# Kernel optimization log

Measured on AMD Instinct MI355X. Metric: run time of the kernel, lower is better.

The kernel has to match this reference:

```python
import jax, jax.numpy as jnp
import numpy as np
import math

D_MODEL = 96
D_STATE = 16
IMG = 32
KSZ = 3
V_LIST = [(0, 0), (0, 1), (0, -1), (1, 0), (-1, 0)]
NUM_V = len(V_LIST)
GROUPS = 4
BATCH = 4


def group_norm(x, gamma, beta, groups=GROUPS, eps=1e-5):
    B, C, H, W = x.shape
    xg = x.reshape(B, groups, C // groups, H, W)
    mu = xg.mean(axis=(2, 3, 4), keepdims=True)
    var = xg.var(axis=(2, 3, 4), keepdims=True)
    xn = ((xg - mu) * jax.lax.rsqrt(var + eps)).reshape(B, C, H, W)
    return xn * gamma[None, :, None, None] + beta[None, :, None, None]


def circ_conv(x, w, b=None):
    # circular padding then VALID conv == padding_mode='circular'
    p = w.shape[-1] // 2
    xp = jnp.pad(x, ((0, 0), (0, 0), (p, p), (p, p)), mode='wrap')
    y = jax.lax.conv_general_dilated(xp, w, (1, 1), 'VALID',
                                     dimension_numbers=('NCHW', 'OIHW', 'NCHW'))
    if b is not None:
        y = y + b[None, :, None, None]
    return y


def setup_inputs() -> dict:
    key = jax.random.key(0)
    ks = jax.random.split(key, 8)
    fan = D_MODEL * KSZ * KSZ
    inp = {
        'u_t': jax.random.normal(ks[0], (BATCH, D_MODEL, IMG, IMG), jnp.float32),
        's_prev': jax.random.normal(ks[1], (BATCH, NUM_V, D_MODEL, D_STATE, IMG, IMG), jnp.float32) * 0.1,
        'gamma': jnp.ones((D_MODEL,), jnp.float32),
        'beta': jnp.zeros((D_MODEL,), jnp.float32),
        'w_delta': jax.random.normal(ks[2], (D_MODEL, D_MODEL, KSZ, KSZ), jnp.float32) / np.sqrt(fan),
        'b_delta': jnp.zeros((D_MODEL,), jnp.float32),
        'w_B': jax.random.normal(ks[3], (D_STATE, D_MODEL, KSZ, KSZ), jnp.float32) / np.sqrt(fan),
        'w_C': jax.random.normal(ks[4], (D_STATE, D_MODEL, KSZ, KSZ), jnp.float32) / np.sqrt(fan),
        'log_A_real': jnp.full((D_MODEL, D_STATE), math.log(0.5), jnp.float32),
        'D_param': jnp.ones((D_MODEL,), jnp.float32),
        'dt_inv_softplus': jnp.asarray(math.log(math.exp(1.0) - 1.0), jnp.float32),
    }
    return inp


def reference(u_t, s_prev, gamma, beta, w_delta, b_delta, w_B, w_C, log_A_real, D_param, dt_inv_softplus):
    B, D, H, W = u_t.shape
    N = D_STATE
    u_norm = group_norm(u_t, gamma, beta)
    delta = jax.nn.softplus(circ_conv(u_norm, w_delta, b_delta) + dt_inv_softplus)
    delta = jnp.clip(delta, 1e-4, 5.0)                          # (B,D,H,W)
    B_val = circ_conv(u_norm, w_B)                               # (B,N,H,W)
    C_val = circ_conv(u_norm, w_C)                               # (B,N,H,W)
    A = -jnp.exp(log_A_real)                                     # (D,N)
    delta_bc = delta[:, :, None]                                 # (B,D,1,H,W)
    A_bar = jnp.exp(delta_bc * A[None, :, :, None, None])        # (B,D,N,H,W)
    B_bar = delta_bc * B_val[:, None]                            # (B,D,N,H,W)
    # flow transport: dest[y,x] = src[(y-vy)%H,(x-vx)%W] == roll by (vy,vx)
    s_tr = jnp.stack([jnp.roll(s_prev[:, i], shift=v, axis=(-2, -1))
                      for i, v in enumerate(V_LIST)], axis=1)    # (B,V,D,N,H,W)
    s_new = A_bar[:, None] * s_tr + B_bar[:, None] * u_t[:, None, :, None]
    y_state = jnp.sum(s_new * C_val[:, None, None], axis=3)      # (B,V,D,H,W)
    y_out = y_state + u_t[:, None] * D_param[None, None, :, None, None]
    return (y_out, s_new)
```

## Files before the change

kernel.cpp:

```cpp
#include <hip/hip_runtime.h>
#include <math.h>

#define D_MODEL 96
#define D_STATE 16
#define IMG 32
#define NUM_V 5
#define GROUPS 4
#define BATCH 4
#define HW (IMG*IMG)
#define CPG (D_MODEL/GROUPS)
#define NCOEF (D_MODEL + 2*D_STATE)
#define Y_SIZE (BATCH*NUM_V*D_MODEL*HW)

__global__ __launch_bounds__(256) void gn_kernel(const float* __restrict__ u,
                                                 const float* __restrict__ gamma,
                                                 const float* __restrict__ beta,
                                                 float* __restrict__ unorm) {
    int b = blockIdx.x >> 2, g = blockIdx.x & 3;
    int t = threadIdx.x;
    const int base = (b * D_MODEL + g * CPG) * HW;
    const int n = CPG * HW;
    float s = 0.f, s2 = 0.f;
    for (int k = t; k < n; k += 256) {
        float v = u[base + k];
        s += v;
        s2 = fmaf(v, v, s2);
    }
    for (int off = 32; off; off >>= 1) {
        s  += __shfl_down(s,  off);
        s2 += __shfl_down(s2, off);
    }
    __shared__ float red[8];
    int wid = t >> 6;
    if ((t & 63) == 0) { red[wid * 2] = s; red[wid * 2 + 1] = s2; }
    __syncthreads();
    if (t == 0) {
        float S = 0.f, S2 = 0.f;
        for (int i = 0; i < 4; ++i) { S += red[i * 2]; S2 += red[i * 2 + 1]; }
        float mu  = S / (float)n;
        float var = S2 / (float)n - mu * mu;
        red[0] = mu;
        red[1] = rsqrtf(var + 1e-5f);
    }
    __syncthreads();
    float mu = red[0], rs = red[1];
    for (int k = t; k < n; k += 256) {
        int c = g * CPG + (k >> 10);
        unorm[base + k] = (u[base + k] - mu) * rs * gamma[c] + beta[c];
    }
}

__global__ __launch_bounds__(256) void conv_kernel(const float* __restrict__ unorm,
                                                   const float* __restrict__ w_delta,
                                                   const float* __restrict__ b_delta,
                                                   const float* __restrict__ w_B,
                                                   const float* __restrict__ w_C,
                                                   const float* __restrict__ dt_ptr,
                                                   float* __restrict__ coef) {
    int bid = blockIdx.x;
    int b  = bid >> 9;
    int oc = (bid >> 2) & 127;
    int hq = bid & 3;
    int t  = threadIdx.x;
    int h  = hq * 8 + (t >> 5);
    int w  = t & 31;
    int lane    = t & 63;
    int rowBase = lane & 32;
    int lsrc = rowBase | ((lane + 31) & 31);
    int rsrc = rowBase | ((lane + 1) & 31);

    const float* wp;
    float bias;
    bool is_delta = false;
    if (oc < D_MODEL) {
        wp = w_delta + oc * D_MODEL * 9;
        bias = b_delta[oc] + dt_ptr[0];
        is_delta = true;
    } else if (oc < D_MODEL + D_STATE) {
        wp = w_B + (oc - D_MODEL) * D_MODEL * 9;
        bias = 0.f;
    } else {
        wp = w_C + (oc - D_MODEL - D_STATE) * D_MODEL * 9;
        bias = 0.f;
    }
    const float* ub = unorm + b * D_MODEL * HW;

    float acc = bias;
    for (int ic = 0; ic < D_MODEL; ++ic) {
        const float* wr = wp + ic * 9;
        const float* ur = ub + ic * HW;
        #pragma unroll
        for (int kh = 0; kh < 3; ++kh) {
            int hh = (h + kh + 31) & 31;
            float c = ur[hh * 32 + w];
            float l = __shfl(c, lsrc);
            float r = __shfl(c, rsrc);
            acc = fmaf(wr[kh * 3 + 0], l, acc);
            acc = fmaf(wr[kh * 3 + 1], c, acc);
            acc = fmaf(wr[kh * 3 + 2], r, acc);
        }
    }
    if (is_delta) {
        float sp = acc > 20.f ? acc : log1pf(__expf(acc));
        acc = fminf(fmaxf(sp, 1e-4f), 5.f);
    }
    coef[(b * NCOEF + oc) * HW + h * 32 + w] = acc;
}

__global__ __launch_bounds__(256) void state_kernel(const float* __restrict__ u_t,
                                                    const float* __restrict__ s_prev,
                                                    const float* __restrict__ coef,
                                                    const float* __restrict__ log_A,
                                                    const float* __restrict__ D_param,
                                                    float* __restrict__ out) {
    int gid = blockIdx.x * 256 + threadIdx.x;
    int b  = gid / (D_MODEL * HW);
    int r  = gid - b * (D_MODEL * HW);
    int d  = r >> 10;
    int hw = r & 1023;
    int h = hw >> 5, w = hw & 31;

    float delta = coef[(b * NCOEF + d) * HW + hw];
    float u     = u_t[(b * D_MODEL + d) * HW + hw];
    float Dp    = D_param[d];

    float Ab[D_STATE], bu[D_STATE], Cv[D_STATE];
    #pragma unroll
    for (int n = 0; n < D_STATE; ++n) {
        float Bv = coef[(b * NCOEF + D_MODEL + n) * HW + hw];
        Cv[n]    = coef[(b * NCOEF + D_MODEL + D_STATE + n) * HW + hw];
        float A  = -__expf(log_A[d * D_STATE + n]);
        Ab[n]    = __expf(delta * A);
        bu[n]    = delta * Bv * u;
    }

    float* out_s = out + Y_SIZE;
    const int vh[NUM_V] = {0, 0, 0, 1, -1};
    const int vw[NUM_V] = {0, 1, -1, 0, 0};
    #pragma unroll
    for (int i = 0; i < NUM_V; ++i) {
        int hs  = (h - vh[i]) & 31;
        int ws  = (w - vw[i]) & 31;
        int hw2 = hs * 32 + ws;
        long sbase = (long)((b * NUM_V + i) * D_MODEL + d) * (D_STATE * HW);
        float y = 0.f;
        #pragma unroll
        for (int n = 0; n < D_STATE; ++n) {
            float s  = s_prev[sbase + n * HW + hw2];
            float sn = fmaf(Ab[n], s, bu[n]);
            out_s[sbase + n * HW + hw] = sn;
            y = fmaf(sn, Cv[n], y);
        }
        out[(long)((b * NUM_V + i) * D_MODEL + d) * HW + hw] = y + u * Dp;
    }
}

extern "C" void kernel_launch(void* const* d_in, const int* in_sizes, int n_in,
                              void* d_out, int out_size, void* d_ws, size_t ws_size,
                              hipStream_t stream) {
    const float* u_t     = (const float*)d_in[0];
    const float* s_prev  = (const float*)d_in[1];
    const float* gamma   = (const float*)d_in[2];
    const float* beta    = (const float*)d_in[3];
    const float* w_delta = (const float*)d_in[4];
    const float* b_delta = (const float*)d_in[5];
    const float* w_B     = (const float*)d_in[6];
    const float* w_C     = (const float*)d_in[7];
    const float* log_A   = (const float*)d_in[8];
    const float* D_param = (const float*)d_in[9];
    const float* dt_ptr  = (const float*)d_in[10];
    float* out = (float*)d_out;

    float* unorm = (float*)d_ws;
    float* coef  = unorm + BATCH * D_MODEL * HW;

    hipLaunchKernelGGL(gn_kernel, dim3(BATCH * GROUPS), dim3(256), 0, stream,
                       u_t, gamma, beta, unorm);
    hipLaunchKernelGGL(conv_kernel, dim3(BATCH * NCOEF * 4), dim3(256), 0, stream,
                       unorm, w_delta, b_delta, w_B, w_C, dt_ptr, coef);
    hipLaunchKernelGGL(state_kernel, dim3(BATCH * D_MODEL * HW / 256), dim3(256), 0, stream,
                       u_t, s_prev, coef, log_A, D_param, out);
}
```

Measured before the change: 354.9 us.

## Vectorize all kernels with float4 loads/stores and nontemporal state writes

Rewrites the group-norm, conv and state kernels to process four adjacent pixels per thread with float4 loads and stores. Horizontal neighbours come from lane shuffles, and the per-state coefficients are computed inside the n loop instead of being held in register arrays. State outputs use nontemporal stores to avoid polluting cache with the large streaming write. The conv grid shrinks to one block per output channel and batch, which cuts parallelism there and makes each thread do four times the work.

```diff
diff --git a/kernel.cpp b/kernel.cpp
--- a/kernel.cpp
+++ b/kernel.cpp
@@ -12,19 +12,26 @@
 #define NCOEF (D_MODEL + 2*D_STATE)
 #define Y_SIZE (BATCH*NUM_V*D_MODEL*HW)
 
-__global__ __launch_bounds__(256) void gn_kernel(const float* __restrict__ u,
+typedef float f32x4 __attribute__((ext_vector_type(4)));
+
+__device__ __forceinline__ void nt_store4(const float4& v, float4* p) {
+    f32x4 tmp = {v.x, v.y, v.z, v.w};
+    __builtin_nontemporal_store(tmp, (f32x4*)p);
+}
+
+__global__ __launch_bounds__(256) void gn_kernel(const float4* __restrict__ u4,
                                                  const float* __restrict__ gamma,
                                                  const float* __restrict__ beta,
-                                                 float* __restrict__ unorm) {
+                                                 float4* __restrict__ unorm4) {
     int b = blockIdx.x >> 2, g = blockIdx.x & 3;
     int t = threadIdx.x;
-    const int base = (b * D_MODEL + g * CPG) * HW;
-    const int n = CPG * HW;
+    const int base4 = ((b * D_MODEL + g * CPG) * HW) >> 2;
+    const int n4 = (CPG * HW) >> 2;
     float s = 0.f, s2 = 0.f;
-    for (int k = t; k < n; k += 256) {
-        float v = u[base + k];
-        s += v;
-        s2 = fmaf(v, v, s2);
+    for (int k = t; k < n4; k += 256) {
+        float4 v = u4[base4 + k];
+        s += v.x + v.y + v.z + v.w;
+        s2 = fmaf(v.x, v.x, fmaf(v.y, v.y, fmaf(v.z, v.z, fmaf(v.w, v.w, s2))));
     }
     for (int off = 32; off; off >>= 1) {
         s  += __shfl_down(s,  off);
@@ -37,37 +44,41 @@
     if (t == 0) {
         float S = 0.f, S2 = 0.f;
         for (int i = 0; i < 4; ++i) { S += red[i * 2]; S2 += red[i * 2 + 1]; }
-        float mu  = S / (float)n;
-        float var = S2 / (float)n - mu * mu;
+        float nf = (float)(CPG * HW);
+        float mu  = S / nf;
+        float var = S2 / nf - mu * mu;
         red[0] = mu;
         red[1] = rsqrtf(var + 1e-5f);
     }
     __syncthreads();
     float mu = red[0], rs = red[1];
-    for (int k = t; k < n; k += 256) {
-        int c = g * CPG + (k >> 10);
-        unorm[base + k] = (u[base + k] - mu) * rs * gamma[c] + beta[c];
-    }
-}
-
-__global__ __launch_bounds__(256) void conv_kernel(const float* __restrict__ unorm,
+    for (int k = t; k < n4; k += 256) {
+        int c = g * CPG + (k >> 8);
+        float ga = gamma[c] * rs, be = beta[c] - mu * gamma[c] * rs;
+        float4 v = u4[base4 + k];
+        float4 o;
+        o.x = fmaf(v.x, ga, be); o.y = fmaf(v.y, ga, be);
+        o.z = fmaf(v.z, ga, be); o.w = fmaf(v.w, ga, be);
+        unorm4[base4 + k] = o;
+    }
+}
+
+__global__ __launch_bounds__(256) void conv_kernel(const float4* __restrict__ unorm4,
                                                    const float* __restrict__ w_delta,
                                                    const float* __restrict__ b_delta,
                                                    const float* __restrict__ w_B,
                                                    const float* __restrict__ w_C,
                                                    const float* __restrict__ dt_ptr,
-                                                   float* __restrict__ coef) {
+                                                   float4* __restrict__ coef4) {
     int bid = blockIdx.x;
-    int b  = bid >> 9;
-    int oc = (bid >> 2) & 127;
-    int hq = bid & 3;
+    int b  = bid >> 7;
+    int oc = bid & 127;
     int t  = threadIdx.x;
-    int h  = hq * 8 + (t >> 5);
-    int w  = t & 31;
-    int lane    = t & 63;
-    int rowBase = lane & 32;
-    int lsrc = rowBase | ((lane + 31) & 31);
-    int rsrc = rowBase | ((lane + 1) & 31);
+    int h  = t >> 3;
+    int j  = t & 7;
+    int lane = t & 63;
+    int ll = (lane & 56) | ((j + 7) & 7);
+    int rl = (lane & 56) | ((j + 1) & 7);
 
     const float* wp;
     float bias;
@@ -83,75 +94,146 @@
         wp = w_C + (oc - D_MODEL - D_STATE) * D_MODEL * 9;
         bias = 0.f;
     }
-    const float* ub = unorm + b * D_MODEL * HW;
-
-    float acc = bias;
+    const float4* ub4 = unorm4 + ((b * D_MODEL * HW) >> 2);
+
+    float4 acc = {bias, bias, bias, bias};
+    int hm = (h + 31) & 31, hp = (h + 1) & 31;
+    int ro[3] = {hm * 8 + j, h * 8 + j, hp * 8 + j};
+
     for (int ic = 0; ic < D_MODEL; ++ic) {
         const float* wr = wp + ic * 9;
-        const float* ur = ub + ic * HW;
+        const int icb = ic * 256;
         #pragma unroll
         for (int kh = 0; kh < 3; ++kh) {
-            int hh = (h + kh + 31) & 31;
-            float c = ur[hh * 32 + w];
-            float l = __shfl(c, lsrc);
-            float r = __shfl(c, rsrc);
-            acc = fmaf(wr[kh * 3 + 0], l, acc);
-            acc = fmaf(wr[kh * 3 + 1], c, acc);
-            acc = fmaf(wr[kh * 3 + 2], r, acc);
+            float4 q = ub4[icb + ro[kh]];
+            float lw = __shfl(q.w, ll);
+            float rx = __shfl(q.x, rl);
+            float wa = wr[kh * 3 + 0], wb = wr[kh * 3 + 1], wc = wr[kh * 3 + 2];
+            acc.x = fmaf(wa, lw,  fmaf(wb, q.x, fmaf(wc, q.y, acc.x)));
+            acc.y = fmaf(wa, q.x, fmaf(wb, q.y, fmaf(wc, q.z, acc.y)));
+            acc.z = fmaf(wa, q.y, fmaf(wb, q.z, fmaf(wc, q.w, acc.z)));
+            acc.w = fmaf(wa, q.z, fmaf(wb, q.w, fmaf(wc, rx,  acc.w)));
         }
     }
     if (is_delta) {
-        float sp = acc > 20.f ? acc : log1pf(__expf(acc));
-        acc = fminf(fmaxf(sp, 1e-4f), 5.f);
-    }
-    coef[(b * NCOEF + oc) * HW + h * 32 + w] = acc;
-}
-
-__global__ __launch_bounds__(256) void state_kernel(const float* __restrict__ u_t,
-                                                    const float* __restrict__ s_prev,
-                                                    const float* __restrict__ coef,
+        float* a = (float*)&acc;
+        #pragma unroll
+        for (int k = 0; k < 4; ++k) {
+            float x = a[k];
+            float sp = x > 20.f ? x : log1pf(__expf(x));
+            a[k] = fminf(fmaxf(sp, 1e-4f), 5.f);
+        }
+    }
+    coef4[((b * NCOEF + oc) * HW >> 2) + h * 8 + j] = acc;
+}
+
+__global__ __launch_bounds__(128) void state_kernel(const float4* __restrict__ u4,
+                                                    const float4* __restrict__ s_prev4,
+                                                    const float4* __restrict__ coef4,
                                                     const float* __restrict__ log_A,
                                                     const float* __restrict__ D_param,
-                                                    float* __restrict__ out) {
-    int gid = blockIdx.x * 256 + threadIdx.x;
-    int b  = gid / (D_MODEL * HW);
-    int r  = gid - b * (D_MODEL * HW);
-    int d  = r >> 10;
-    int hw = r & 1023;
-    int h = hw >> 5, w = hw & 31;
-
-    float delta = coef[(b * NCOEF + d) * HW + hw];
-    float u     = u_t[(b * D_MODEL + d) * HW + hw];
-    float Dp    = D_param[d];
-
-    float Ab[D_STATE], bu[D_STATE], Cv[D_STATE];
+                                                    float4* __restrict__ out4) {
+    int bid = blockIdx.x;
+    int b = bid / 192;
+    int r = bid - b * 192;
+    int d = r >> 1;
+    int half = r & 1;
+    int t = threadIdx.x;
+    int h = half * 16 + (t >> 3);
+    int j = t & 7;
+    int lane = t & 63;
+    int ll = (lane & 56) | ((j + 7) & 7);
+    int rl = (lane & 56) | ((j + 1) & 7);
+    int hw4 = h * 8 + j;
+
+    float4 delta = coef4[((b * NCOEF + d) * HW >> 2) + hw4];
+    float4 u     = u4[((b * D_MODEL + d) * HW >> 2) + hw4];
+    float Dp     = D_param[d];
+    const float* lA = log_A + d * D_STATE;
+
+    int pb[NUM_V];
     #pragma unroll
+    for (int i = 0; i < NUM_V; ++i)
+        pb[i] = ((b * NUM_V + i) * D_MODEL + d) * (D_STATE * HW / 4);
+    int hm4 = (((h + 31) & 31) * 8) + j;
+    int hp4 = (((h + 1) & 31) * 8) + j;
+
+    float4* outs4 = out4 + (Y_SIZE >> 2);
+
+    float4 y0 = {0,0,0,0}, y1 = {0,0,0,0}, y2 = {0,0,0,0}, y3 = {0,0,0,0}, y4v = {0,0,0,0};
+
+    #pragma unroll 2
     for (int n = 0; n < D_STATE; ++n) {
-        float Bv = coef[(b * NCOEF + D_MODEL + n) * HW + hw];
-        Cv[n]    = coef[(b * NCOEF + D_MODEL + D_STATE + n) * HW + hw];
-        float A  = -__expf(log_A[d * D_STATE + n]);
-        Ab[n]    = __expf(delta * A);
-        bu[n]    = delta * Bv * u;
-    }
-
-    float* out_s = out + Y_SIZE;
-    const int vh[NUM_V] = {0, 0, 0, 1, -1};
-    const int vw[NUM_V] = {0, 1, -1, 0, 0};
+        int n4 = n * (HW / 4);
+        float4 Bv = coef4[((b * NCOEF + D_MODEL + n) * HW >> 2) + hw4];
+        float4 Cv = coef4[((b * NCOEF + D_MODEL + D_STATE + n) * HW >> 2) + hw4];
+        float A = -__expf(lA[n]);
+        float4 Ab, bu;
+        Ab.x = __expf(delta.x * A); Ab.y = __expf(delta.y * A);
+        Ab.z = __expf(delta.z * A); Ab.w = __expf(delta.w * A);
+        bu.x = delta.x * Bv.x * u.x; bu.y = delta.y * Bv.y * u.y;
+        bu.z = delta.z * Bv.z * u.z; bu.w = delta.w * Bv.w * u.w;
+
+        {
+            float4 s = s_prev4[pb[0] + n4 + hw4];
+            float4 sn;
+            sn.x = fmaf(Ab.x, s.x, bu.x); sn.y = fmaf(Ab.y, s.y, bu.y);
+            sn.z = fmaf(Ab.z, s.z, bu.z); sn.w = fmaf(Ab.w, s.w, bu.w);
+            nt_store4(sn, &outs4[pb[0] + n4 + hw4]);
+            y0.x = fmaf(sn.x, Cv.x, y0.x); y0.y = fmaf(sn.y, Cv.y, y0.y);
+            y0.z = fmaf(sn.z, Cv.z, y0.z); y0.w = fmaf(sn.w, Cv.w, y0.w);
+        }
+        {
+            float4 q = s_prev4[pb[1] + n4 + hw4];
+            float lw = __shfl(q.w, ll);
+            float4 s = {lw, q.x, q.y, q.z};
+            float4 sn;
+            sn.x = fmaf(Ab.x, s.x, bu.x); sn.y = fmaf(Ab.y, s.y, bu.y);
+            sn.z = fmaf(Ab.z, s.z, bu.z); sn.w = fmaf(Ab.w, s.w, bu.w);
+            nt_store4(sn, &outs4[pb[1] + n4 + hw4]);
+            y1.x = fmaf(sn.x, Cv.x, y1.x); y1.y = fmaf(sn.y, Cv.y, y1.y);
+            y1.z = fmaf(sn.z, Cv.z, y1.z); y1.w = fmaf(sn.w, Cv.w, y1.w);
+        }
+        {
+            float4 q = s_prev4[pb[2] + n4 + hw4];
+            float rx = __shfl(q.x, rl);
+            float4 s = {q.y, q.z, q.w, rx};
+            float4 sn;
+            sn.x = fmaf(Ab.x, s.x, bu.x); sn.y = fmaf(Ab.y, s.y, bu.y);
+            sn.z = fmaf(Ab.z, s.z, bu.z); sn.w = fmaf(Ab.w, s.w, bu.w);
+            nt_store4(sn, &outs4[pb[2] + n4 + hw4]);
+            y2.x = fmaf(sn.x, Cv.x, y2.x); y2.y = fmaf(sn.y, Cv.y, y2.y);
+            y2.z = fmaf(sn.z, Cv.z, y2.z); y2.w = fmaf(sn.w, Cv.w, y2.w);
+        }
+        {
+            float4 s = s_prev4[pb[3] + n4 + hm4];
+            float4 sn;
+            sn.x = fmaf(Ab.x, s.x, bu.x); sn.y = fmaf(Ab.y, s.y, bu.y);
+            sn.z = fmaf(Ab.z, s.z, bu.z); sn.w = fmaf(Ab.w, s.w, bu.w);
+            nt_store4(sn, &outs4[pb[3] + n4 + hw4]);
+            y3.x = fmaf(sn.x, Cv.x, y3.x); y3.y = fmaf(sn.y, Cv.y, y3.y);
+            y3.z = fmaf(sn.z, Cv.z, y3.z); y3.w = fmaf(sn.w, Cv.w, y3.w);
+        }
+        {
+            float4 s = s_prev4[pb[4] + n4 + hp4];
+            float4 sn;
+            sn.x = fmaf(Ab.x, s.x, bu.x); sn.y = fmaf(Ab.y, s.y, bu.y);
+            sn.z = fmaf(Ab.z, s.z, bu.z); sn.w = fmaf(Ab.w, s.w, bu.w);
+            nt_store4(sn, &outs4[pb[4] + n4 + hw4]);
+            y4v.x = fmaf(sn.x, Cv.x, y4v.x); y4v.y = fmaf(sn.y, Cv.y, y4v.y);
+            y4v.z = fmaf(sn.z, Cv.z, y4v.z); y4v.w = fmaf(sn.w, Cv.w, y4v.w);
+        }
+    }
+
+    float4 du;
+    du.x = u.x * Dp; du.y = u.y * Dp; du.z = u.z * Dp; du.w = u.w * Dp;
+    float4* yy[NUM_V] = {&y0, &y1, &y2, &y3, &y4v};
     #pragma unroll
     for (int i = 0; i < NUM_V; ++i) {
-        int hs  = (h - vh[i]) & 31;
-        int ws  = (w - vw[i]) & 31;
-        int hw2 = hs * 32 + ws;
-        long sbase = (long)((b * NUM_V + i) * D_MODEL + d) * (D_STATE * HW);
-        float y = 0.f;
-        #pragma unroll
-        for (int n = 0; n < D_STATE; ++n) {
-            float s  = s_prev[sbase + n * HW + hw2];
-            float sn = fmaf(Ab[n], s, bu[n]);
-            out_s[sbase + n * HW + hw] = sn;
-            y = fmaf(sn, Cv[n], y);
-        }
-        out[(long)((b * NUM_V + i) * D_MODEL + d) * HW + hw] = y + u * Dp;
+        float4 o;
+        o.x = yy[i]->x + du.x; o.y = yy[i]->y + du.y;
+        o.z = yy[i]->z + du.z; o.w = yy[i]->w + du.w;
+        out4[(((b * NUM_V + i) * D_MODEL + d) * HW >> 2) + hw4] = o;
     }
 }
 
@@ -175,9 +257,11 @@
     float* coef  = unorm + BATCH * D_MODEL * HW;
 
     hipLaunchKernelGGL(gn_kernel, dim3(BATCH * GROUPS), dim3(256), 0, stream,
-                       u_t, gamma, beta, unorm);
-    hipLaunchKernelGGL(conv_kernel, dim3(BATCH * NCOEF * 4), dim3(256), 0, stream,
-                       unorm, w_delta, b_delta, w_B, w_C, dt_ptr, coef);
-    hipLaunchKernelGGL(state_kernel, dim3(BATCH * D_MODEL * HW / 256), dim3(256), 0, stream,
-                       u_t, s_prev, coef, log_A, D_param, out);
-}
+                       (const float4*)u_t, gamma, beta, (float4*)unorm);
+    hipLaunchKernelGGL(conv_kernel, dim3(BATCH * NCOEF), dim3(256), 0, stream,
+                       (const float4*)unorm, w_delta, b_delta, w_B, w_C, dt_ptr,
+                       (float4*)coef);
+    hipLaunchKernelGGL(state_kernel, dim3(768), dim3(128), 0, stream,
+                       (const float4*)u_t, (const float4*)s_prev, (const float4*)coef,
+                       log_A, D_param, (float4*)out);
+}
```

After: 310.2 us. -12.6%, faster.
